# Kernel optimization log

Measured on AMD Instinct MI355X. Metric: run time of the kernel, lower is better.

Reference implementation:

```python
import jax, jax.numpy as jnp
import numpy as np

C = 64  # in_channels == out_channels (required by final view)

def setup_inputs() -> dict:
    key = jax.random.key(0)
    ks = jax.random.split(key, 7)
    x = jax.random.normal(ks[0], (2, C, 16, 16, 16), dtype=jnp.float32)
    s = 1.0 / np.sqrt(C)
    Wq = jax.random.uniform(ks[1], (C, C), jnp.float32, -s, s)
    bq = jax.random.uniform(ks[2], (C,), jnp.float32, -s, s)
    Wk = jax.random.uniform(ks[3], (C, C), jnp.float32, -s, s)
    bk = jax.random.uniform(ks[4], (C,), jnp.float32, -s, s)
    Wv = jax.random.uniform(ks[5], (C, C), jnp.float32, -s, s)
    bv = jax.random.uniform(ks[6], (C,), jnp.float32, -s, s)
    return {"x": x, "Wq": Wq, "bq": bq, "Wk": Wk, "bk": bk, "Wv": Wv, "bv": bv}

def _proj(x, W, b):
    # 1x1x1 Conv3d == per-voxel channel GEMM; x: [B,C,D,H,W]
    return jnp.einsum('oc,bcdhw->bodhw', W, x) + b[None, :, None, None, None]

def reference(x, Wq, bq, Wk, bk, Wv, bv):
    B, Cin, D, H, W = x.shape
    q = _proj(x, Wq, bq).reshape(B, C, -1)  # [B,C,N]
    k = _proj(x, Wk, bk).reshape(B, C, -1)
    v = _proj(x, Wv, bv).reshape(B, C, -1)
    # attention[b,i,j] = softmax_j(q_i . k_j); NOTE: unscaled, as in the source
    attn = jax.nn.softmax(jnp.einsum('bci,bcj->bij', q, k), axis=-1)
    out = jnp.einsum('bcj,bij->bci', v, attn)  # out_i = sum_j a_ij v_j
    return out.reshape(x.shape)
```

## Files before the change

kernel.cpp:

```cpp
#include <hip/hip_runtime.h>
#include <math.h>

#define CCH 64
#define NVOX 4096
#define NB 2
#define SMAX 16.0f

typedef _Float16 f16x8 __attribute__((ext_vector_type(8)));
typedef _Float16 f16x4 __attribute__((ext_vector_type(4)));
typedef __fp16   g16x2 __attribute__((ext_vector_type(2)));
typedef float f32x4 __attribute__((ext_vector_type(4)));

__device__ __forceinline__ void gload_lds16(const void* g, void* l) {
    __builtin_amdgcn_global_load_lds(
        (const __attribute__((address_space(1))) unsigned int*)g,
        (__attribute__((address_space(3))) unsigned int*)l,
        16, 0, 0);
}

__global__ __launch_bounds__(256) void qkv_proj(
    const float* __restrict__ x,
    const float* __restrict__ Wq, const float* __restrict__ bq,
    const float* __restrict__ Wk, const float* __restrict__ bk,
    const float* __restrict__ Wv, const float* __restrict__ bv,
    _Float16* __restrict__ qh, _Float16* __restrict__ khf, _Float16* __restrict__ vhf,
    float* __restrict__ lsum, float* __restrict__ out)
{
    __shared__ float Ws[3 * 64 * 64];
    __shared__ float xs[64 * 32];
    const int t  = threadIdx.x;
    const int b  = blockIdx.x >> 7;
    const int i0 = (blockIdx.x & 127) * 32;

    {
        const float4 z = make_float4(0.f, 0.f, 0.f, 0.f);
        float4* o4 = (float4*)out;
        o4[(size_t)blockIdx.x * 512 + t * 2]     = z;
        o4[(size_t)blockIdx.x * 512 + t * 2 + 1] = z;
        if (t < 32) lsum[blockIdx.x * 32 + t] = 0.f;
    }

    {
        const float4* Wq4 = (const float4*)Wq;
        const float4* Wk4 = (const float4*)Wk;
        const float4* Wv4 = (const float4*)Wv;
        float4* Ws4 = (float4*)Ws;
#pragma unroll
        for (int s = 0; s < 4; ++s) {
            int idx = t + 256 * s;
            Ws4[idx]        = Wq4[idx];
            Ws4[1024 + idx] = Wk4[idx];
            Ws4[2048 + idx] = Wv4[idx];
        }
    }
    {
        int cc = t >> 2;
        int m0 = (t & 3) * 8;
        const float4* s4 = (const float4*)(x + ((b * CCH + cc) * NVOX) + i0 + m0);
        float4* x4 = (float4*)&xs[cc * 32 + m0];
        x4[0] = s4[0];
        x4[1] = s4[1];
    }
    __syncthreads();

    const int vox = t & 31;
    const int c0  = (t >> 5) * 8;
    const int j   = i0 + vox;
    const int jb  = j >> 4;

#pragma unroll
    for (int m = 0; m < 3; ++m) {
        const float* Wm  = &Ws[m * 4096];
        const float* bia = (m == 0) ? bq : (m == 1) ? bk : bv;
        float acc[8];
#pragma unroll
        for (int jj = 0; jj < 8; ++jj) acc[jj] = bia[c0 + jj];
        for (int cc = 0; cc < 64; cc += 4) {
            float xv0 = xs[(cc + 0) * 32 + vox];
            float xv1 = xs[(cc + 1) * 32 + vox];
            float xv2 = xs[(cc + 2) * 32 + vox];
            float xv3 = xs[(cc + 3) * 32 + vox];
#pragma unroll
            for (int jj = 0; jj < 8; ++jj) {
                float4 w = *(const float4*)&Wm[(c0 + jj) * 64 + cc];
                acc[jj] = fmaf(w.x, xv0, acc[jj]);
                acc[jj] = fmaf(w.y, xv1, acc[jj]);
                acc[jj] = fmaf(w.z, xv2, acc[jj]);
                acc[jj] = fmaf(w.w, xv3, acc[jj]);
            }
        }
        if (m == 0) {
            f16x8 hv;
#pragma unroll
            for (int jj = 0; jj < 8; ++jj) hv[jj] = (_Float16)acc[jj];
            *(f16x8*)&qh[((size_t)(b * NVOX) + j) * CCH + c0] = hv;
        } else if (m == 1) {
            f16x8 hv;
#pragma unroll
            for (int jj = 0; jj < 8; ++jj) hv[jj] = (_Float16)acc[jj];
            const int ks = c0 >> 5, q4 = (c0 >> 3) & 3, n = j & 15;
            *(f16x8*)&khf[((((size_t)b * 256 + jb) * 2 + ks) * 64 + q4 * 16 + n) * 8] = hv;
        } else {
            const int q4v = (j >> 2) & 3, r = j & 3;
#pragma unroll
            for (int jj = 0; jj < 8; ++jj) {
                const int c = c0 + jj, mt = c >> 4, nch = c & 15;
                vhf[((((size_t)b * 256 + jb) * 4 + mt) * 64 + q4v * 16 + nch) * 4 + r] =
                    (_Float16)acc[jj];
            }
        }
    }
}

__global__ __launch_bounds__(256, 2) void attn8(
    const _Float16* __restrict__ qh, const _Float16* __restrict__ khf,
    const _Float16* __restrict__ vhf,
    float* __restrict__ lsum,
    float* __restrict__ out)
{
    constexpr int JT = 8;
    __shared__ __align__(16) _Float16 skv[4][8192];

    const int t    = threadIdx.x;
    const int h    = blockIdx.x & 7;
    const int tile = blockIdx.x >> 3;
    const int b    = tile >> 5;
    const int i0   = (tile & 31) * 128;

    const int lane = t & 63;
    const int w    = t >> 6;
    const int q4   = lane >> 4;
    const int n    = lane & 15;

    const size_t jbB = ((size_t)b * 256 + h * 32) * 2048;

    f16x8 aq[2][2];
#pragma unroll
    for (int g = 0; g < 2; ++g) {
        const _Float16* qrow =
            qh + ((size_t)(b * NVOX) + i0 + w * 32 + g * 16 + n) * CCH + q4 * 8;
        aq[g][0] = *(const f16x8*)(qrow);
        aq[g][1] = *(const f16x8*)(qrow + 32);
    }

    float l[2] = {0.f, 0.f};
    f32x4 o[2][4];
#pragma unroll
    for (int g = 0; g < 2; ++g)
#pragma unroll
        for (int mt = 0; mt < 4; ++mt) o[g][mt] = (f32x4){0.f, 0.f, 0.f, 0.f};

    auto STAGE = [&](int jt, int buf) {
        const char* gk = (const char*)khf + jbB + (size_t)jt * 8192 + w * 2048 + lane * 16;
        const char* gv = (const char*)vhf + jbB + (size_t)jt * 8192 + w * 2048 + lane * 16;
        char* lk = (char*)&skv[buf][0]    + w * 2048;
        char* lv = (char*)&skv[buf][4096] + w * 2048;
        gload_lds16(gk,        lk);
        gload_lds16(gk + 1024, lk + 1024);
        gload_lds16(gv,        lv);
        gload_lds16(gv + 1024, lv + 1024);
    };

    STAGE(0, 0);
    STAGE(1, 1);

#pragma unroll
    for (int jt = 0; jt < JT; ++jt) {
        const int buf = jt & 3;
        if (jt + 2 < JT) STAGE(jt + 2, (jt + 2) & 3);
        if (jt + 2 < JT)      { asm volatile("s_waitcnt vmcnt(8)" ::: "memory"); }
        else if (jt + 1 < JT) { asm volatile("s_waitcnt vmcnt(4)" ::: "memory"); }
        else                  { asm volatile("s_waitcnt vmcnt(0)" ::: "memory"); }
        __builtin_amdgcn_s_barrier();
        __builtin_amdgcn_sched_barrier(0);

        f16x8 ak[2][4];
        f16x4 av[4][4];
        {
            const f16x8* k8 = (const f16x8*)&skv[buf][0];
            const f16x4* v4 = (const f16x4*)&skv[buf][4096];
#pragma unroll
            for (int nt = 0; nt < 4; ++nt) {
                ak[0][nt] = k8[(nt * 2 + 0) * 64 + lane];
                ak[1][nt] = k8[(nt * 2 + 1) * 64 + lane];
            }
#pragma unroll
            for (int nt = 0; nt < 4; ++nt)
#pragma unroll
                for (int mt = 0; mt < 4; ++mt)
                    av[nt][mt] = v4[(nt * 4 + mt) * 64 + lane];
        }

        f32x4 s[2][4];
#pragma unroll
        for (int g = 0; g < 2; ++g)
#pragma unroll
            for (int nt = 0; nt < 4; ++nt) s[g][nt] = (f32x4){0.f, 0.f, 0.f, 0.f};
#pragma unroll
        for (int ks = 0; ks < 2; ++ks)
#pragma unroll
            for (int nt = 0; nt < 4; ++nt) {
                s[0][nt] = __builtin_amdgcn_mfma_f32_16x16x32_f16(ak[ks][nt], aq[0][ks], s[0][nt], 0, 0, 0);
                s[1][nt] = __builtin_amdgcn_mfma_f32_16x16x32_f16(ak[ks][nt], aq[1][ks], s[1][nt], 0, 0, 0);
            }

        f16x4 bp[2][4];
#pragma unroll
        for (int g = 0; g < 2; ++g) {
#pragma unroll
            for (int nt = 0; nt < 4; ++nt) {
                float p0 = __expf(s[g][nt][0] - SMAX);
                float p1 = __expf(s[g][nt][1] - SMAX);
                float p2 = __expf(s[g][nt][2] - SMAX);
                float p3 = __expf(s[g][nt][3] - SMAX);
                l[g] += (p0 + p1) + (p2 + p3);
                union { g16x2 g2[2]; f16x4 h4; } u;
                u.g2[0] = __builtin_amdgcn_cvt_pkrtz(p0, p1);
                u.g2[1] = __builtin_amdgcn_cvt_pkrtz(p2, p3);
                bp[g][nt] = u.h4;
            }
        }

#pragma unroll
        for (int nt = 0; nt < 4; ++nt)
#pragma unroll
            for (int mt = 0; mt < 4; ++mt) {
                o[0][mt] = __builtin_amdgcn_mfma_f32_16x16x16f16(av[nt][mt], bp[0][nt], o[0][mt], 0, 0, 0);
                o[1][mt] = __builtin_amdgcn_mfma_f32_16x16x16f16(av[nt][mt], bp[1][nt], o[1][mt], 0, 0, 0);
            }
    }

    float l_tot[2];
#pragma unroll
    for (int g = 0; g < 2; ++g) {
        float lv = l[g];
        lv += __shfl_xor(lv, 16, 64);
        lv += __shfl_xor(lv, 32, 64);
        l_tot[g] = lv;
    }

#pragma unroll
    for (int g = 0; g < 2; ++g) {
        const int ig = i0 + w * 32 + g * 16 + n;
        if (q4 == 0) atomicAdd(&lsum[(size_t)b * NVOX + ig], l_tot[g]);
#pragma unroll
        for (int mt = 0; mt < 4; ++mt)
#pragma unroll
            for (int r = 0; r < 4; ++r)
                atomicAdd(&out[(size_t)(b * CCH + mt * 16 + q4 * 4 + r) * NVOX + ig],
                          o[g][mt][r]);
    }
}

__global__ __launch_bounds__(256) void norm_out(
    const float* __restrict__ lsum, float* __restrict__ out)
{
    const int t  = threadIdx.x;
    const int b  = blockIdx.x >> 7;
    const int i0 = (blockIdx.x & 127) * 32 + (t & 3) * 8;
    const int c  = t >> 2;

    float inv[8];
#pragma unroll
    for (int e = 0; e < 8; ++e) inv[e] = 1.0f / lsum[(size_t)b * NVOX + i0 + e];

    float4* p = (float4*)&out[(size_t)(b * CCH + c) * NVOX + i0];
    float4 a = p[0], d = p[1];
    a.x *= inv[0]; a.y *= inv[1]; a.z *= inv[2]; a.w *= inv[3];
    d.x *= inv[4]; d.y *= inv[5]; d.z *= inv[6]; d.w *= inv[7];
    p[0] = a; p[1] = d;
}

extern "C" void kernel_launch(void* const* d_in, const int* in_sizes, int n_in,
                              void* d_out, int out_size, void* d_ws, size_t ws_size,
                              hipStream_t stream)
{
    const float* x  = (const float*)d_in[0];
    const float* Wq = (const float*)d_in[1];
    const float* bq = (const float*)d_in[2];
    const float* Wk = (const float*)d_in[3];
    const float* bk = (const float*)d_in[4];
    const float* Wv = (const float*)d_in[5];
    const float* bv = (const float*)d_in[6];
    float* out = (float*)d_out;

    _Float16* qh  = (_Float16*)d_ws;
    _Float16* khf = qh + NB * NVOX * CCH;
    _Float16* vhf = khf + NB * NVOX * CCH;
    float*    lsum = (float*)(vhf + NB * NVOX * CCH);

    qkv_proj<<<NB * (NVOX / 32), 256, 0, stream>>>(x, Wq, bq, Wk, bk, Wv, bv,
                                                   qh, khf, vhf, lsum, out);
    attn8<<<NB * 32 * 8, 256, 0, stream>>>(qh, khf, vhf, lsum, out);
    norm_out<<<NB * 128, 256, 0, stream>>>(lsum, out);
}
```

Baseline: 100.6 us.

## Fuse normalization into attention via last-block ticket and use 512-thread blocks

Drops the separate norm_out kernel. Each query tile now keeps a per-tile atomic counter, and the last of the 8 split-K blocks to finish reads the accumulated lsum and out and writes the normalized result. Blocks grow to 512 threads covering 256 queries, so each wave stages half as much K/V per tile and the grid shrinks. This saves one kernel launch and one extra pass over the output, in exchange for a serialized tail in the last block per tile, atomic fences, and fewer blocks in flight.

```diff
diff --git a/kernel.cpp b/kernel.cpp
--- a/kernel.cpp
+++ b/kernel.cpp
@@ -24,7 +24,7 @@
     const float* __restrict__ Wk, const float* __restrict__ bk,
     const float* __restrict__ Wv, const float* __restrict__ bv,
     _Float16* __restrict__ qh, _Float16* __restrict__ khf, _Float16* __restrict__ vhf,
-    float* __restrict__ lsum, float* __restrict__ out)
+    float* __restrict__ lsum, int* __restrict__ cnt, float* __restrict__ out)
 {
     __shared__ float Ws[3 * 64 * 64];
     __shared__ float xs[64 * 32];
@@ -38,6 +38,7 @@
         o4[(size_t)blockIdx.x * 512 + t * 2]     = z;
         o4[(size_t)blockIdx.x * 512 + t * 2 + 1] = z;
         if (t < 32) lsum[blockIdx.x * 32 + t] = 0.f;
+        if (blockIdx.x == 0 && t < 32) cnt[t] = 0;
     }
 
     {
@@ -112,20 +113,23 @@
     }
 }
 
-__global__ __launch_bounds__(256, 2) void attn8(
+__global__ __launch_bounds__(512, 2) void attn8(
     const _Float16* __restrict__ qh, const _Float16* __restrict__ khf,
     const _Float16* __restrict__ vhf,
     float* __restrict__ lsum,
+    int* __restrict__ cnt,
     float* __restrict__ out)
 {
     constexpr int JT = 8;
     __shared__ __align__(16) _Float16 skv[4][8192];
+    __shared__ float invs[256];
+    __shared__ int tick;
 
     const int t    = threadIdx.x;
     const int h    = blockIdx.x & 7;
     const int tile = blockIdx.x >> 3;
-    const int b    = tile >> 5;
-    const int i0   = (tile & 31) * 128;
+    const int b    = tile >> 4;
+    const int i0   = (tile & 15) * 256;
 
     const int lane = t & 63;
     const int w    = t >> 6;
@@ -151,14 +155,12 @@
         for (int mt = 0; mt < 4; ++mt) o[g][mt] = (f32x4){0.f, 0.f, 0.f, 0.f};
 
     auto STAGE = [&](int jt, int buf) {
-        const char* gk = (const char*)khf + jbB + (size_t)jt * 8192 + w * 2048 + lane * 16;
-        const char* gv = (const char*)vhf + jbB + (size_t)jt * 8192 + w * 2048 + lane * 16;
-        char* lk = (char*)&skv[buf][0]    + w * 2048;
-        char* lv = (char*)&skv[buf][4096] + w * 2048;
-        gload_lds16(gk,        lk);
-        gload_lds16(gk + 1024, lk + 1024);
-        gload_lds16(gv,        lv);
-        gload_lds16(gv + 1024, lv + 1024);
+        const char* gk = (const char*)khf + jbB + (size_t)jt * 8192 + w * 1024 + lane * 16;
+        const char* gv = (const char*)vhf + jbB + (size_t)jt * 8192 + w * 1024 + lane * 16;
+        char* lk = (char*)&skv[buf][0]    + w * 1024;
+        char* lv = (char*)&skv[buf][4096] + w * 1024;
+        gload_lds16(gk, lk);
+        gload_lds16(gv, lv);
     };
 
     STAGE(0, 0);
@@ -168,8 +170,8 @@
     for (int jt = 0; jt < JT; ++jt) {
         const int buf = jt & 3;
         if (jt + 2 < JT) STAGE(jt + 2, (jt + 2) & 3);
-        if (jt + 2 < JT)      { asm volatile("s_waitcnt vmcnt(8)" ::: "memory"); }
-        else if (jt + 1 < JT) { asm volatile("s_waitcnt vmcnt(4)" ::: "memory"); }
+        if (jt + 2 < JT)      { asm volatile("s_waitcnt vmcnt(4)" ::: "memory"); }
+        else if (jt + 1 < JT) { asm volatile("s_waitcnt vmcnt(2)" ::: "memory"); }
         else                  { asm volatile("s_waitcnt vmcnt(0)" ::: "memory"); }
         __builtin_amdgcn_s_barrier();
         __builtin_amdgcn_sched_barrier(0);
@@ -250,25 +252,32 @@
                 atomicAdd(&out[(size_t)(b * CCH + mt * 16 + q4 * 4 + r) * NVOX + ig],
                           o[g][mt][r]);
     }
-}
-
-__global__ __launch_bounds__(256) void norm_out(
-    const float* __restrict__ lsum, float* __restrict__ out)
-{
-    const int t  = threadIdx.x;
-    const int b  = blockIdx.x >> 7;
-    const int i0 = (blockIdx.x & 127) * 32 + (t & 3) * 8;
-    const int c  = t >> 2;
-
-    float inv[8];
-#pragma unroll
-    for (int e = 0; e < 8; ++e) inv[e] = 1.0f / lsum[(size_t)b * NVOX + i0 + e];
-
-    float4* p = (float4*)&out[(size_t)(b * CCH + c) * NVOX + i0];
-    float4 a = p[0], d = p[1];
-    a.x *= inv[0]; a.y *= inv[1]; a.z *= inv[2]; a.w *= inv[3];
-    d.x *= inv[4]; d.y *= inv[5]; d.z *= inv[6]; d.w *= inv[7];
-    p[0] = a; p[1] = d;
+
+    asm volatile("s_waitcnt vmcnt(0)" ::: "memory");
+    __syncthreads();
+    if (t == 0) {
+        __threadfence();
+        tick = __hip_atomic_fetch_add(&cnt[tile], 1, __ATOMIC_ACQ_REL,
+                                      __HIP_MEMORY_SCOPE_AGENT);
+    }
+    __syncthreads();
+
+    if (tick == 7) {
+        if (t < 256) {
+            float lv = __hip_atomic_load(&lsum[(size_t)b * NVOX + i0 + t],
+                                         __ATOMIC_RELAXED, __HIP_MEMORY_SCOPE_AGENT);
+            invs[t] = 1.0f / lv;
+        }
+        __syncthreads();
+        const int c  = t >> 3;
+        const int r0 = (t & 7) * 32;
+        float* op = &out[(size_t)(b * CCH + c) * NVOX + i0 + r0];
+#pragma unroll
+        for (int e = 0; e < 32; ++e) {
+            float v = __hip_atomic_load(&op[e], __ATOMIC_RELAXED, __HIP_MEMORY_SCOPE_AGENT);
+            op[e] = v * invs[r0 + e];
+        }
+    }
 }
 
 extern "C" void kernel_launch(void* const* d_in, const int* in_sizes, int n_in,
@@ -288,9 +297,9 @@
     _Float16* khf = qh + NB * NVOX * CCH;
     _Float16* vhf = khf + NB * NVOX * CCH;
     float*    lsum = (float*)(vhf + NB * NVOX * CCH);
+    int*      cnt  = (int*)(lsum + NB * NVOX);
 
     qkv_proj<<<NB * (NVOX / 32), 256, 0, stream>>>(x, Wq, bq, Wk, bk, Wv, bv,
-                                                   qh, khf, vhf, lsum, out);
-    attn8<<<NB * 32 * 8, 256, 0, stream>>>(qh, khf, vhf, lsum, out);
-    norm_out<<<NB * 128, 256, 0, stream>>>(lsum, out);
+                                                   qh, khf, vhf, lsum, cnt, out);
+    attn8<<<NB * 16 * 8, 512, 0, stream>>>(qh, khf, vhf, lsum, cnt, out);
 }
```

After: 136.9 us. 1.36x slower.
